# Kernel optimization log

Measured on AMD Instinct MI355X. Metric: run time of the kernel, lower is better.

Reference implementation:

```python
import jax, jax.numpy as jnp
import numpy as np

N, E = 50000, 800000
IN_C, HID_C, OUT_C, HEADS = 128, 32, 16, 4
NEG_SLOPE = 0.2


def gat_conv(x, src, dst, W, att_src, att_dst, bias, heads, out_ch, concat, n_nodes):
    # linear transform: [N, heads, out_ch]
    h = (x @ W).reshape(n_nodes, heads, out_ch)
    # per-node attention logits [N, heads]
    a_s = (h * att_src).sum(-1)
    a_d = (h * att_dst).sum(-1)
    # per-edge raw attention (edge j->i uses src logit of j, dst logit of i)
    alpha = jax.nn.leaky_relu(a_s[src] + a_d[dst], negative_slope=NEG_SLOPE)  # [E, heads]
    # segment softmax over destination neighborhoods
    amax = jax.ops.segment_max(alpha, dst, num_segments=n_nodes)
    ex = jnp.exp(alpha - amax[dst])
    den = jax.ops.segment_sum(ex, dst, num_segments=n_nodes)
    coef = ex / den[dst]  # [E, heads]
    # weighted scatter-add aggregation
    msg = h[src] * coef[:, :, None]  # [E, heads, out_ch]
    out = jax.ops.segment_sum(msg, dst, num_segments=n_nodes)  # [N, heads, out_ch]
    out = out.reshape(n_nodes, heads * out_ch) if concat else out.mean(axis=1)
    return out + bias


def setup_inputs() -> dict:
    key = jax.random.key(0)
    ks = jax.random.split(key, 10)
    x = jax.random.normal(ks[0], (N, IN_C), dtype=jnp.float32)
    edge_index = jax.random.randint(ks[1], (2, E), 0, N, dtype=jnp.int64)
    s1 = 1.0 / np.sqrt(IN_C)
    s2 = 1.0 / np.sqrt(HID_C * HEADS)
    W1 = jax.random.normal(ks[2], (IN_C, HEADS * HID_C), dtype=jnp.float32) * s1
    att_src1 = jax.random.normal(ks[3], (HEADS, HID_C), dtype=jnp.float32) * s1
    att_dst1 = jax.random.normal(ks[4], (HEADS, HID_C), dtype=jnp.float32) * s1
    b1 = jnp.zeros((HEADS * HID_C,), dtype=jnp.float32)
    W2 = jax.random.normal(ks[5], (HEADS * HID_C, OUT_C), dtype=jnp.float32) * s2
    att_src2 = jax.random.normal(ks[6], (1, OUT_C), dtype=jnp.float32) * s2
    att_dst2 = jax.random.normal(ks[7], (1, OUT_C), dtype=jnp.float32) * s2
    b2 = jnp.zeros((OUT_C,), dtype=jnp.float32)
    return {"x": x, "edge_index": edge_index, "W1": W1, "att_src1": att_src1,
            "att_dst1": att_dst1, "b1": b1, "W2": W2, "att_src2": att_src2,
            "att_dst2": att_dst2, "b2": b2}


def reference(x, edge_index, W1, att_src1, att_dst1, b1, W2, att_src2, att_dst2, b2):
    n = x.shape[0]
    # PyG GATConv default: add self loops
    ar = jnp.arange(n, dtype=edge_index.dtype)
    src = jnp.concatenate([edge_index[0], ar])
    dst = jnp.concatenate([edge_index[1], ar])
    h = gat_conv(x, src, dst, W1, att_src1, att_dst1, b1, HEADS, HID_C, True, n)
    h = jax.nn.elu(h)
    out = gat_conv(h, src, dst, W2, att_src2, att_dst2, b2, 1, OUT_C, False, n)
    return out
```

## Files before the change

### kernel.cpp

```cpp
#include <hip/hip_runtime.h>

typedef __attribute__((ext_vector_type(8))) short short8;
typedef __attribute__((ext_vector_type(4))) float f32x4;
typedef __attribute__((ext_vector_type(2))) float f32x2;

__device__ __forceinline__ float lrelu02(float a) { return a > 0.0f ? a : 0.2f * a; }

__device__ __forceinline__ unsigned bf16rne(float f) {
    unsigned u = __float_as_uint(f);
    return (u + 0x7fffu + ((u >> 16) & 1u)) >> 16;
}

__global__ __launch_bounds__(256) void k_rank(
    const int* __restrict__ ei, int* __restrict__ deg, int* __restrict__ rank, int E)
{
    int tid = blockIdx.x * blockDim.x + threadIdx.x;
    int nthr = gridDim.x * blockDim.x;
    int E4 = E & ~3;
    for (int b = tid * 4; b < E4; b += nthr * 4) {
        int4 d = *(const int4*)(ei + E + b);
        int4 r;
        r.x = atomicAdd(&deg[d.x], 1);
        r.y = atomicAdd(&deg[d.y], 1);
        r.z = atomicAdd(&deg[d.z], 1);
        r.w = atomicAdd(&deg[d.w], 1);
        *(int4*)(rank + b) = r;
    }
    for (int e = E4 + tid; e < E; e += nthr)
        rank[e] = atomicAdd(&deg[ei[E + e]], 1);
}

__global__ __launch_bounds__(256) void k_gemm1(
    const float* __restrict__ x, const float* __restrict__ W,
    const float* __restrict__ attS, const float* __restrict__ attD,
    unsigned short* __restrict__ h1, float* __restrict__ as1, float* __restrict__ ad1,
    int4* __restrict__ degz, int n4, int N)
{
    __shared__ unsigned short Wt[128 * 128];
    __shared__ unsigned short xs[64 * 128];

    const int t = threadIdx.x;
    const int lane = t & 63;
    const int wv = t >> 6;
    const int ln = lane & 15;
    const int lg = lane >> 4;
    const int r0 = blockIdx.x * 64;

    for (int i = blockIdx.x * 256 + t; i < n4; i += gridDim.x * 256)
        degz[i] = make_int4(0, 0, 0, 0);

    #pragma unroll
    for (int i = 0; i < 16; ++i) {
        int flat = i * 256 + t;
        int n = flat & 127;
        int k0 = (flat >> 7) * 4;
        float v0 = W[(size_t)(k0 + 0) * 128 + n];
        float v1 = W[(size_t)(k0 + 1) * 128 + n];
        float v2 = W[(size_t)(k0 + 2) * 128 + n];
        float v3 = W[(size_t)(k0 + 3) * 128 + n];
        uint2 pk;
        pk.x = bf16rne(v0) | (bf16rne(v1) << 16);
        pk.y = bf16rne(v2) | (bf16rne(v3) << 16);
        int byteo = n * 256 + ((k0 * 2) ^ ((n & 7) << 4));
        *(uint2*)((char*)Wt + byteo) = pk;
    }
    {
        int mbase = t >> 5, k0 = (t & 31) * 4;
        #pragma unroll
        for (int it = 0; it < 8; ++it) {
            int m = mbase + it * 8;
            int rr = r0 + m;
            float4 v = make_float4(0.f, 0.f, 0.f, 0.f);
            if (rr < N) v = *(const float4*)&x[(size_t)rr * 128 + k0];
            unsigned lo = bf16rne(v.x) | (bf16rne(v.y) << 16);
            unsigned hi = bf16rne(v.z) | (bf16rne(v.w) << 16);
            int byteo = m * 256 + ((k0 * 2) ^ ((m & 7) << 4));
            *(uint2*)((char*)xs + byteo) = make_uint2(lo, hi);
        }
    }
    __syncthreads();

    f32x4 acc[8];
    #pragma unroll
    for (int i = 0; i < 8; ++i) acc[i] = (f32x4)(0.f);

    #pragma unroll
    for (int kk = 0; kk < 4; ++kk) {
        int kb = (kk * 32 + lg * 8) * 2;
        int am = wv * 16 + ln;
        short8 a = *(const short8*)((char*)xs + am * 256 + (kb ^ ((am & 7) << 4)));
        #pragma unroll
        for (int tile = 0; tile < 8; ++tile) {
            int n = tile * 16 + ln;
            short8 b = *(const short8*)((char*)Wt + n * 256 + (kb ^ ((n & 7) << 4)));
            acc[tile] = __builtin_amdgcn_mfma_f32_16x16x32_bf16(a, b, acc[tile], 0, 0, 0);
        }
    }

    float aSt[8], aDt[8];
    #pragma unroll
    for (int tile = 0; tile < 8; ++tile) {
        aSt[tile] = attS[tile * 16 + ln];
        aDt[tile] = attD[tile * 16 + ln];
    }
    #pragma unroll
    for (int r = 0; r < 4; ++r) {
        int row = r0 + wv * 16 + lg * 4 + r;
        #pragma unroll
        for (int h = 0; h < 4; ++h) {
            float s = acc[2*h][r] * aSt[2*h] + acc[2*h+1][r] * aSt[2*h+1];
            float d = acc[2*h][r] * aDt[2*h] + acc[2*h+1][r] * aDt[2*h+1];
            s += __shfl_xor(s, 1); s += __shfl_xor(s, 2); s += __shfl_xor(s, 4); s += __shfl_xor(s, 8);
            d += __shfl_xor(d, 1); d += __shfl_xor(d, 2); d += __shfl_xor(d, 4); d += __shfl_xor(d, 8);
            if (ln == h * 4 + r && row < N) {
                as1[row * 4 + h] = s;
                ad1[row * 4 + h] = d;
            }
        }
    }

    __syncthreads();
    #pragma unroll
    for (int tile = 0; tile < 8; ++tile) {
        #pragma unroll
        for (int r = 0; r < 4; ++r) {
            int m = wv * 16 + lg * 4 + r;
            int byteo = m * 256 + (((tile * 16 + ln) * 2) ^ ((m & 7) << 4));
            *(unsigned short*)((char*)xs + byteo) = (unsigned short)bf16rne(acc[tile][r]);
        }
    }
    __syncthreads();
    #pragma unroll
    for (int it = 0; it < 4; ++it) {
        int idx = t + it * 256;
        int m = idx >> 4, o = idx & 15;
        int byteo = m * 256 + ((o * 16) ^ ((m & 7) << 4));
        if (r0 + m < N)
            *(uint4*)((char*)(h1 + (size_t)(r0 + m) * 128) + o * 16) =
                *(const uint4*)((const char*)xs + byteo);
    }
}

__global__ __launch_bounds__(256) void k_scan_local(
    const int* __restrict__ deg, int* __restrict__ rowptr, int* __restrict__ bsum, int N)
{
    const int t = threadIdx.x;
    const int base = blockIdx.x * 2048 + t * 8;
    int v[8];
    int s = 0;
    #pragma unroll
    for (int j = 0; j < 8; ++j) {
        int idx = base + j;
        v[j] = (idx < N) ? deg[idx] : 0;
        s += v[j];
    }
    __shared__ int ts[256];
    ts[t] = s;
    __syncthreads();
    #pragma unroll
    for (int off = 1; off < 256; off <<= 1) {
        int u = (t >= off) ? ts[t - off] : 0;
        __syncthreads();
        ts[t] += u;
        __syncthreads();
    }
    int ex = (t == 0) ? 0 : ts[t - 1];
    #pragma unroll
    for (int j = 0; j < 8; ++j) {
        int idx = base + j;
        if (idx < N) rowptr[idx] = ex;
        ex += v[j];
    }
    if (t == 255) bsum[blockIdx.x] = ts[255];
}

__global__ __launch_bounds__(256) void k_scan_add(
    int* __restrict__ rowptr, const int* __restrict__ bsum, int N, int E)
{
    const int t = threadIdx.x;
    __shared__ int soff;
    if (t < 64) {
        int v = (t < (int)blockIdx.x) ? bsum[t] : 0;
        #pragma unroll
        for (int m = 32; m >= 1; m >>= 1) v += __shfl_xor(v, m);
        if (t == 0) soff = v;
    }
    __syncthreads();
    int off = soff;
    const int base = blockIdx.x * 2048 + t * 8;
    #pragma unroll
    for (int j = 0; j < 8; ++j) {
        int idx = base + j;
        if (idx < N) rowptr[idx] += off;
    }
    if (blockIdx.x == 0 && t == 0) rowptr[N] = E;
}

__global__ __launch_bounds__(256) void k_fill2(const int* __restrict__ ei,
                                               const int* __restrict__ rank,
                                               const int* __restrict__ rowptr,
                                               int* __restrict__ col, int E) {
    int tid = blockIdx.x * blockDim.x + threadIdx.x;
    int nthr = gridDim.x * blockDim.x;
    int E4 = E & ~3;
    for (int b = tid * 4; b < E4; b += nthr * 4) {
        int4 d = *(const int4*)(ei + E + b);
        int4 s = *(const int4*)(ei + b);
        int4 r = *(const int4*)(rank + b);
        col[rowptr[d.x] + r.x] = s.x;
        col[rowptr[d.y] + r.y] = s.y;
        col[rowptr[d.z] + r.z] = s.z;
        col[rowptr[d.w] + r.w] = s.w;
    }
    for (int e = E4 + tid; e < E; e += nthr)
        col[rowptr[ei[E + e]] + rank[e]] = ei[e];
}

__global__ __launch_bounds__(256) void k_agg1(
    const unsigned short* __restrict__ h1, const float* __restrict__ as1,
    const float* __restrict__ ad1, const int* __restrict__ rowptr,
    const int* __restrict__ col, const float* __restrict__ b1,
    unsigned short* __restrict__ out1, int N)
{
    int wid = (int)(((unsigned)blockIdx.x * blockDim.x + threadIdx.x) >> 6);
    if (wid >= N) return;
    int lane = threadIdx.x & 63;
    int start = rowptr[wid], end = rowptr[wid + 1];
    int deg = end - start;
    const float4 ad = *(const float4*)(ad1 + (size_t)wid * 4);
    int head = lane >> 4;
    float adh = head == 0 ? ad.x : head == 1 ? ad.y : head == 2 ? ad.z : ad.w;

    float aself = as1[(size_t)wid * 4 + head];
    float vself = __expf(lrelu02(aself + adh));
    unsigned hvs = *(const unsigned*)(h1 + (size_t)wid * 128 + lane * 2);

    f32x2 acc2 = (f32x2)(0.f);

    if (deg <= 64) {
        int idx = lane & 15;
        float ex[4];
        int sv[4];
        float den = 0.f;
        #pragma unroll
        for (int b = 0; b < 4; ++b) {
            int j = b * 16 + idx;
            float v = 0.f;
            int sc = 0;
            if (j < deg) {
                sc = col[start + j];
                v = __expf(lrelu02(as1[(size_t)sc * 4 + head] + adh));
            }
            sv[b] = sc;
            ex[b] = v;
            den += v;
        }
        den += __shfl_xor(den, 1); den += __shfl_xor(den, 2);
        den += __shfl_xor(den, 4); den += __shfl_xor(den, 8);
        den += vself;
        float rden = 1.f / den;
        #pragma unroll
        for (int b = 0; b < 4; ++b) ex[b] *= rden;
        {
            float cs = vself * rden;
            f32x2 hs;
            hs.x = __uint_as_float(hvs << 16);
            hs.y = __uint_as_float(hvs & 0xffff0000u);
            acc2 += (f32x2)(cs) * hs;
        }
        int srcbase = lane & 48;

        #pragma unroll
        for (int b = 0; b < 4; ++b) {
            int rem = deg - b * 16;
            if (rem <= 0) break;
            if (rem >= 16) {
                int sq[16]; float cf[16]; unsigned hv[16];
                #pragma unroll
                for (int q = 0; q < 16; ++q) {
                    sq[q] = __builtin_amdgcn_readlane(sv[b], q);
                    cf[q] = __shfl(ex[b], srcbase | q);
                }
                #pragma unroll
                for (int q = 0; q < 16; ++q)
                    hv[q] = *(const unsigned*)(h1 + (size_t)sq[q] * 128 + lane * 2);
                #pragma unroll
                for (int q = 0; q < 16; ++q) {
                    f32x2 h2v;
                    h2v.x = __uint_as_float(hv[q] << 16);
                    h2v.y = __uint_as_float(hv[q] & 0xffff0000u);
                    acc2 += (f32x2)(cf[q]) * h2v;
                }
            } else {
                #pragma unroll
                for (int c4 = 0; c4 < 4; ++c4) {
                    if (c4 * 4 >= rem) break;
                    int sq[4]; float cf[4]; unsigned hv[4];
                    #pragma unroll
                    for (int jj = 0; jj < 4; ++jj) {
                        int q = c4 * 4 + jj;
                        sq[jj] = __builtin_amdgcn_readlane(sv[b], q);
                        cf[jj] = __shfl(ex[b], srcbase | q);
                    }
                    #pragma unroll
                    for (int jj = 0; jj < 4; ++jj)
                        hv[jj] = *(const unsigned*)(h1 + (size_t)sq[jj] * 128 + lane * 2);
                    #pragma unroll
                    for (int jj = 0; jj < 4; ++jj) {
                        f32x2 h2v;
                        h2v.x = __uint_as_float(hv[jj] << 16);
                        h2v.y = __uint_as_float(hv[jj] & 0xffff0000u);
                        acc2 += (f32x2)(cf[jj]) * h2v;
                    }
                }
            }
        }
    } else {
        float den0 = 0.f, den1 = 0.f, den2 = 0.f, den3 = 0.f;
        for (int e = start + lane; e < end; e += 64) {
            int src = col[e];
            const float4 a = *(const float4*)(as1 + (size_t)src * 4);
            den0 += __expf(lrelu02(a.x + ad.x));
            den1 += __expf(lrelu02(a.y + ad.y));
            den2 += __expf(lrelu02(a.z + ad.z));
            den3 += __expf(lrelu02(a.w + ad.w));
        }
        #pragma unroll
        for (int m = 32; m >= 1; m >>= 1) {
            den0 += __shfl_xor(den0, m); den1 += __shfl_xor(den1, m);
            den2 += __shfl_xor(den2, m); den3 += __shfl_xor(den3, m);
        }
        const float4 asf = *(const float4*)(as1 + (size_t)wid * 4);
        den0 += __expf(lrelu02(asf.x + ad.x));
        den1 += __expf(lrelu02(asf.y + ad.y));
        den2 += __expf(lrelu02(asf.z + ad.z));
        den3 += __expf(lrelu02(asf.w + ad.w));
        float rden = head == 0 ? 1.f/den0 : head == 1 ? 1.f/den1 : head == 2 ? 1.f/den2 : 1.f/den3;
        {
            float cs = vself * rden;
            f32x2 hs;
            hs.x = __uint_as_float(hvs << 16);
            hs.y = __uint_as_float(hvs & 0xffff0000u);
            acc2 += (f32x2)(cs) * hs;
        }
        for (int e = start; e < end; e += 8) {
            int sq[8]; float av[8], km[8]; unsigned hv[8];
            #pragma unroll
            for (int j = 0; j < 8; ++j) {
                int ee = e + j;
                bool ok = ee < end;
                int es = ok ? ee : e;
                sq[j] = __builtin_amdgcn_readfirstlane(col[es]);
                km[j] = ok ? 1.f : 0.f;
            }
            #pragma unroll
            for (int j = 0; j < 8; ++j)
                av[j] = as1[(size_t)sq[j] * 4 + head];
            #pragma unroll
            for (int j = 0; j < 8; ++j)
                hv[j] = *(const unsigned*)(h1 + (size_t)sq[j] * 128 + lane * 2);
            #pragma unroll
            for (int j = 0; j < 8; ++j) {
                float coef = km[j] * __expf(lrelu02(av[j] + adh)) * rden;
                f32x2 h2v;
                h2v.x = __uint_as_float(hv[j] << 16);
                h2v.y = __uint_as_float(hv[j] & 0xffff0000u);
                acc2 += (f32x2)(coef) * h2v;
            }
        }
    }

    int c0 = lane * 2;
    float o0 = acc2.x + b1[c0];
    float o1 = acc2.y + b1[c0 + 1];
    o0 = o0 > 0.f ? o0 : expm1f(o0);
    o1 = o1 > 0.f ? o1 : expm1f(o1);
    unsigned ov = bf16rne(o0) | (bf16rne(o1) << 16);
    *(unsigned*)((char*)out1 + (size_t)wid * 256 + lane * 4) = ov;
}

__global__ __launch_bounds__(256) void k_gemm2(
    const unsigned short* __restrict__ in, const float* __restrict__ W,
    const float* __restrict__ attS, const float* __restrict__ attD,
    float* __restrict__ h2, float* __restrict__ as2, float* __restrict__ ad2, int N)
{
    __shared__ unsigned short Wt[16 * 128];
    __shared__ unsigned short xs[64 * 128];
    const int t = threadIdx.x;
    const int lane = t & 63;
    const int wv = t >> 6;
    const int ln = lane & 15;
    const int lg = lane >> 4;
    const int r0 = blockIdx.x * 64;

    #pragma unroll
    for (int i = 0; i < 2; ++i) {
        int flat = i * 256 + t;
        int n = flat & 15;
        int k0 = (flat >> 4) * 4;
        float v0 = W[(size_t)(k0 + 0) * 16 + n];
        float v1 = W[(size_t)(k0 + 1) * 16 + n];
        float v2 = W[(size_t)(k0 + 2) * 16 + n];
        float v3 = W[(size_t)(k0 + 3) * 16 + n];
        uint2 pk;
        pk.x = bf16rne(v0) | (bf16rne(v1) << 16);
        pk.y = bf16rne(v2) | (bf16rne(v3) << 16);
        int byteo = n * 256 + ((k0 * 2) ^ ((n & 7) << 4));
        *(uint2*)((char*)Wt + byteo) = pk;
    }
    #pragma unroll
    for (int it = 0; it < 4; ++it) {
        int idx = t + it * 256;
        int m = idx >> 4, o = idx & 15;
        int rr = r0 + m;
        uint4 v = make_uint4(0, 0, 0, 0);
        if (rr < N) v = *(const uint4*)((const char*)(in + (size_t)rr * 128) + o * 16);
        int byteo = m * 256 + ((o * 16) ^ ((m & 7) << 4));
        *(uint4*)((char*)xs + byteo) = v;
    }
    __syncthreads();

    f32x4 acc = (f32x4)(0.f);
    #pragma unroll
    for (int kk = 0; kk < 4; ++kk) {
        int kb = (kk * 32 + lg * 8) * 2;
        int am = wv * 16 + ln;
        short8 a = *(const short8*)((char*)xs + am * 256 + (kb ^ ((am & 7) << 4)));
        short8 b = *(const short8*)((char*)Wt + ln * 256 + (kb ^ ((ln & 7) << 4)));
        acc = __builtin_amdgcn_mfma_f32_16x16x32_bf16(a, b, acc, 0, 0, 0);
    }

    float aSv = attS[ln], aDv = attD[ln];
    #pragma unroll
    for (int r = 0; r < 4; ++r) {
        int row = r0 + wv * 16 + lg * 4 + r;
        float s = acc[r] * aSv;
        float d = acc[r] * aDv;
        s += __shfl_xor(s, 1); s += __shfl_xor(s, 2); s += __shfl_xor(s, 4); s += __shfl_xor(s, 8);
        d += __shfl_xor(d, 1); d += __shfl_xor(d, 2); d += __shfl_xor(d, 4); d += __shfl_xor(d, 8);
        if (row < N) {
            h2[(size_t)row * 16 + ln] = acc[r];
            if (ln == 0) { as2[row] = s; ad2[row] = d; }
        }
    }
}

__global__ __launch_bounds__(256) void k_agg2(
    const float* __restrict__ h2, const float* __restrict__ as2,
    const float* __restrict__ ad2, const int* __restrict__ rowptr,
    const int* __restrict__ col, const float* __restrict__ b2,
    float* __restrict__ out, int N)
{
    int wid = (int)(((unsigned)blockIdx.x * blockDim.x + threadIdx.x) >> 6);
    if (wid >= N) return;
    int lane = threadIdx.x & 63;
    int start = rowptr[wid], end = rowptr[wid + 1];
    int deg = end - start;
    float adv = ad2[wid];
    int sub = lane >> 4, c = lane & 15;
    float vself = __expf(lrelu02(as2[wid] + adv));
    float acc = 0.f;

    if (deg <= 64) {
        float ex0 = 0.f;
        if (lane < deg) ex0 = __expf(lrelu02(as2[col[start + lane]] + adv));
        float den = ex0;
        #pragma unroll
        for (int m = 32; m >= 1; m >>= 1) den += __shfl_xor(den, m);
        den += vself;
        float rden = 1.f / den;
        ex0 *= rden;
        if (sub == 0) acc = fmaf(vself * rden, h2[(size_t)wid * 16 + c], acc);
        #pragma unroll
        for (int g = 0; g < 4; ++g) {
            if (g * 16 >= deg) break;
            int s[4]; float cf[4], hv[4];
            #pragma unroll
            for (int jj = 0; jj < 4; ++jj) {
                int j = g * 16 + jj * 4 + sub;
                s[jj]  = col[start + (j < deg ? j : 0)];
                cf[jj] = __shfl(ex0, j);
            }
            #pragma unroll
            for (int jj = 0; jj < 4; ++jj)
                hv[jj] = h2[(size_t)s[jj] * 16 + c];
            #pragma unroll
            for (int jj = 0; jj < 4; ++jj)
                acc = fmaf(cf[jj], hv[jj], acc);
        }
    } else {
        float den = 0.f;
        for (int e = start + lane; e < end; e += 64)
            den += __expf(lrelu02(as2[col[e]] + adv));
        #pragma unroll
        for (int m = 32; m >= 1; m >>= 1) den += __shfl_xor(den, m);
        den += vself;
        float rden = 1.f / den;
        if (sub == 0) acc = fmaf(vself * rden, h2[(size_t)wid * 16 + c], acc);
        for (int e0 = start + sub; e0 < end; e0 += 16) {
            int s[4]; float av[4], km[4], hv[4];
            #pragma unroll
            for (int jj = 0; jj < 4; ++jj) {
                int ee = e0 + jj * 4;
                bool ok = ee < end;
                int es = ok ? ee : e0;
                s[jj]  = col[es];
                km[jj] = ok ? 1.f : 0.f;
            }
            #pragma unroll
            for (int jj = 0; jj < 4; ++jj)
                av[jj] = as2[s[jj]];
            #pragma unroll
            for (int jj = 0; jj < 4; ++jj)
                hv[jj] = h2[(size_t)s[jj] * 16 + c];
            #pragma unroll
            for (int jj = 0; jj < 4; ++jj) {
                float coef = km[jj] * __expf(lrelu02(av[jj] + adv)) * rden;
                acc = fmaf(coef, hv[jj], acc);
            }
        }
    }

    acc += __shfl_xor(acc, 16);
    acc += __shfl_xor(acc, 32);
    if (lane < 16) out[(size_t)wid * 16 + lane] = acc + b2[lane];
}

extern "C" void kernel_launch(void* const* d_in, const int* in_sizes, int n_in,
                              void* d_out, int out_size, void* d_ws, size_t ws_size,
                              hipStream_t stream)
{
    const float* x   = (const float*)d_in[0];
    const int*   ei  = (const int*)d_in[1];
    const float* W1  = (const float*)d_in[2];
    const float* aS1 = (const float*)d_in[3];
    const float* aD1 = (const float*)d_in[4];
    const float* b1  = (const float*)d_in[5];
    const float* W2  = (const float*)d_in[6];
    const float* aS2 = (const float*)d_in[7];
    const float* aD2 = (const float*)d_in[8];
    const float* b2  = (const float*)d_in[9];
    float* out = (float*)d_out;

    int N = in_sizes[0] / 128;
    int E = in_sizes[1] / 2;
    int nblk = (N + 2047) / 2048;
    int G1 = (N + 63) / 64;

    char* w = (char*)d_ws;
    auto alloc = [&](size_t bytes) -> void* {
        void* p = (void*)w;
        w += (bytes + 255) & ~(size_t)255;
        return p;
    };
    unsigned short* h1   = (unsigned short*)alloc((size_t)N * 128 * 2);
    unsigned short* out1 = (unsigned short*)alloc((size_t)N * 128 * 2);
    float* as1   = (float*)alloc((size_t)N * 4 * 4);
    float* ad1   = (float*)alloc((size_t)N * 4 * 4);
    float* h2    = (float*)alloc((size_t)N * 16 * 4);
    float* as2v  = (float*)alloc((size_t)N * 4);
    float* ad2v  = (float*)alloc((size_t)N * 4);
    int* deg     = (int*)alloc((size_t)(N + 4) * 4);
    int* rowptr  = (int*)alloc((size_t)(N + 1) * 4);
    int* rank    = (int*)alloc((size_t)E * 4);
    int* col     = (int*)alloc((size_t)E * 4);
    int* bsum    = (int*)alloc(64 * 4);

    const int tb = 256;
    int n4 = (N + 3) / 4;

    k_gemm1<<<G1, tb, 0, stream>>>(x, W1, aS1, aD1, h1, as1, ad1,
                                   (int4*)deg, n4, N);
    k_rank <<<2048, tb, 0, stream>>>(ei, deg, rank, E);
    k_scan_local<<<nblk, tb, 0, stream>>>(deg, rowptr, bsum, N);
    k_scan_add  <<<nblk, tb, 0, stream>>>(rowptr, bsum, N, E);
    k_fill2<<<1024, tb, 0, stream>>>(ei, rank, rowptr, col, E);

    k_agg1 <<<(N + 3) / 4, tb, 0, stream>>>(h1, as1, ad1, rowptr, col, b1, out1, N);
    k_gemm2<<<G1, tb, 0, stream>>>(out1, W2, aS2, aD2, h2, as2v, ad2v, N);
    k_agg2 <<<(N + 3) / 4, tb, 0, stream>>>(h2, as2v, ad2v, rowptr, col, b2, out, N);
}
```

Baseline: 150.1 us.

## Fuse CSR build stages into one kernel with inter-block flag synchronization

```diff
diff --git a/kernel.cpp b/kernel.cpp
--- a/kernel.cpp
+++ b/kernel.cpp
@@ -11,30 +11,127 @@
     return (u + 0x7fffu + ((u >> 16) & 1u)) >> 16;
 }
 
-__global__ __launch_bounds__(256) void k_rank(
-    const int* __restrict__ ei, int* __restrict__ deg, int* __restrict__ rank, int E)
+__device__ __forceinline__ void waitflag(int* f, int target) {
+    while (__hip_atomic_load(f, __ATOMIC_ACQUIRE, __HIP_MEMORY_SCOPE_AGENT) < target)
+        __builtin_amdgcn_s_sleep(8);
+}
+
+__global__ __launch_bounds__(256, 8) void k_csr(
+    const int* __restrict__ ei, int* __restrict__ deg, int* __restrict__ rank,
+    int* __restrict__ rowptr, int* __restrict__ bsum, int* __restrict__ col,
+    int* __restrict__ flags, int E, int N, int RB, int SB)
 {
-    int tid = blockIdx.x * blockDim.x + threadIdx.x;
-    int nthr = gridDim.x * blockDim.x;
-    int E4 = E & ~3;
-    for (int b = tid * 4; b < E4; b += nthr * 4) {
-        int4 d = *(const int4*)(ei + E + b);
-        int4 r;
-        r.x = atomicAdd(&deg[d.x], 1);
-        r.y = atomicAdd(&deg[d.y], 1);
-        r.z = atomicAdd(&deg[d.z], 1);
-        r.w = atomicAdd(&deg[d.w], 1);
-        *(int4*)(rank + b) = r;
-    }
-    for (int e = E4 + tid; e < E; e += nthr)
-        rank[e] = atomicAdd(&deg[ei[E + e]], 1);
+    const int t = threadIdx.x;
+    const int b = blockIdx.x;
+
+    if (b < RB) {
+        int tid = b * 256 + t;
+        int nthr = RB * 256;
+        int E4 = E & ~3;
+        for (int e = tid * 4; e < E4; e += nthr * 4) {
+            int4 d = *(const int4*)(ei + E + e);
+            int4 r;
+            r.x = atomicAdd(&deg[d.x], 1);
+            r.y = atomicAdd(&deg[d.y], 1);
+            r.z = atomicAdd(&deg[d.z], 1);
+            r.w = atomicAdd(&deg[d.w], 1);
+            *(int4*)(rank + e) = r;
+        }
+        for (int e = E4 + tid; e < E; e += nthr)
+            rank[e] = atomicAdd(&deg[ei[E + e]], 1);
+        __syncthreads();
+        if (t == 0) {
+            __threadfence();
+            __hip_atomic_fetch_add(&flags[0], 1, __ATOMIC_RELEASE, __HIP_MEMORY_SCOPE_AGENT);
+        }
+        return;
+    }
+
+    if (b < RB + SB) {
+        const int sb = b - RB;
+        if (t == 0) waitflag(&flags[0], RB);
+        __syncthreads();
+
+        const int base = sb * 2048 + t * 8;
+        int v[8];
+        int s = 0;
+        #pragma unroll
+        for (int j = 0; j < 8; ++j) {
+            int idx = base + j;
+            v[j] = (idx < N) ? deg[idx] : 0;
+            s += v[j];
+        }
+        __shared__ int ts[256];
+        ts[t] = s;
+        __syncthreads();
+        #pragma unroll
+        for (int off = 1; off < 256; off <<= 1) {
+            int u = (t >= off) ? ts[t - off] : 0;
+            __syncthreads();
+            ts[t] += u;
+            __syncthreads();
+        }
+        int myex = (t == 0) ? 0 : ts[t - 1];
+        if (t == 255) bsum[sb] = ts[255];
+        __syncthreads();
+        if (t == 0) {
+            __threadfence();
+            __hip_atomic_fetch_add(&flags[1], 1, __ATOMIC_RELEASE, __HIP_MEMORY_SCOPE_AGENT);
+            waitflag(&flags[1], SB);
+        }
+        __syncthreads();
+
+        __shared__ int soff;
+        if (t < 64) {
+            int u = (t < sb) ? bsum[t] : 0;
+            #pragma unroll
+            for (int m = 32; m >= 1; m >>= 1) u += __shfl_xor(u, m);
+            if (t == 0) soff = u;
+        }
+        __syncthreads();
+        int run = soff + myex;
+        #pragma unroll
+        for (int j = 0; j < 8; ++j) {
+            int idx = base + j;
+            if (idx < N) rowptr[idx] = run;
+            run += v[j];
+        }
+        if (sb == 0 && t == 0) rowptr[N] = E;
+        __syncthreads();
+        if (t == 0) {
+            __threadfence();
+            __hip_atomic_fetch_add(&flags[2], 1, __ATOMIC_RELEASE, __HIP_MEMORY_SCOPE_AGENT);
+        }
+        return;
+    }
+
+    if (t == 0) waitflag(&flags[2], SB);
+    __syncthreads();
+    {
+        int fb = b - RB - SB;
+        int FB = gridDim.x - RB - SB;
+        int tid = fb * 256 + t;
+        int nthr = FB * 256;
+        int E4 = E & ~3;
+        for (int e = tid * 4; e < E4; e += nthr * 4) {
+            int4 d = *(const int4*)(ei + E + e);
+            int4 sv = *(const int4*)(ei + e);
+            int4 r = *(const int4*)(rank + e);
+            col[rowptr[d.x] + r.x] = sv.x;
+            col[rowptr[d.y] + r.y] = sv.y;
+            col[rowptr[d.z] + r.z] = sv.z;
+            col[rowptr[d.w] + r.w] = sv.w;
+        }
+        for (int e = E4 + tid; e < E; e += nthr)
+            col[rowptr[ei[E + e]] + rank[e]] = ei[e];
+    }
 }
 
 __global__ __launch_bounds__(256) void k_gemm1(
     const float* __restrict__ x, const float* __restrict__ W,
     const float* __restrict__ attS, const float* __restrict__ attD,
     unsigned short* __restrict__ h1, float* __restrict__ as1, float* __restrict__ ad1,
-    int4* __restrict__ degz, int n4, int N)
+    int4* __restrict__ degz, int* __restrict__ flags, int n4, int N)
 {
     __shared__ unsigned short Wt[128 * 128];
     __shared__ unsigned short xs[64 * 128];
@@ -48,6 +145,7 @@
 
     for (int i = blockIdx.x * 256 + t; i < n4; i += gridDim.x * 256)
         degz[i] = make_int4(0, 0, 0, 0);
+    if (blockIdx.x == 0 && t < 8) flags[t] = 0;
 
     #pragma unroll
     for (int i = 0; i < 16; ++i) {
@@ -139,81 +237,6 @@
             *(uint4*)((char*)(h1 + (size_t)(r0 + m) * 128) + o * 16) =
                 *(const uint4*)((const char*)xs + byteo);
     }
-}
-
-__global__ __launch_bounds__(256) void k_scan_local(
-    const int* __restrict__ deg, int* __restrict__ rowptr, int* __restrict__ bsum, int N)
-{
-    const int t = threadIdx.x;
-    const int base = blockIdx.x * 2048 + t * 8;
-    int v[8];
-    int s = 0;
-    #pragma unroll
-    for (int j = 0; j < 8; ++j) {
-        int idx = base + j;
-        v[j] = (idx < N) ? deg[idx] : 0;
-        s += v[j];
-    }
-    __shared__ int ts[256];
-    ts[t] = s;
-    __syncthreads();
-    #pragma unroll
-    for (int off = 1; off < 256; off <<= 1) {
-        int u = (t >= off) ? ts[t - off] : 0;
-        __syncthreads();
-        ts[t] += u;
-        __syncthreads();
-    }
-    int ex = (t == 0) ? 0 : ts[t - 1];
-    #pragma unroll
-    for (int j = 0; j < 8; ++j) {
-        int idx = base + j;
-        if (idx < N) rowptr[idx] = ex;
-        ex += v[j];
-    }
-    if (t == 255) bsum[blockIdx.x] = ts[255];
-}
-
-__global__ __launch_bounds__(256) void k_scan_add(
-    int* __restrict__ rowptr, const int* __restrict__ bsum, int N, int E)
-{
-    const int t = threadIdx.x;
-    __shared__ int soff;
-    if (t < 64) {
-        int v = (t < (int)blockIdx.x) ? bsum[t] : 0;
-        #pragma unroll
-        for (int m = 32; m >= 1; m >>= 1) v += __shfl_xor(v, m);
-        if (t == 0) soff = v;
-    }
-    __syncthreads();
-    int off = soff;
-    const int base = blockIdx.x * 2048 + t * 8;
-    #pragma unroll
-    for (int j = 0; j < 8; ++j) {
-        int idx = base + j;
-        if (idx < N) rowptr[idx] += off;
-    }
-    if (blockIdx.x == 0 && t == 0) rowptr[N] = E;
-}
-
-__global__ __launch_bounds__(256) void k_fill2(const int* __restrict__ ei,
-                                               const int* __restrict__ rank,
-                                               const int* __restrict__ rowptr,
-                                               int* __restrict__ col, int E) {
-    int tid = blockIdx.x * blockDim.x + threadIdx.x;
-    int nthr = gridDim.x * blockDim.x;
-    int E4 = E & ~3;
-    for (int b = tid * 4; b < E4; b += nthr * 4) {
-        int4 d = *(const int4*)(ei + E + b);
-        int4 s = *(const int4*)(ei + b);
-        int4 r = *(const int4*)(rank + b);
-        col[rowptr[d.x] + r.x] = s.x;
-        col[rowptr[d.y] + r.y] = s.y;
-        col[rowptr[d.z] + r.z] = s.z;
-        col[rowptr[d.w] + r.w] = s.w;
-    }
-    for (int e = E4 + tid; e < E; e += nthr)
-        col[rowptr[ei[E + e]] + rank[e]] = ei[e];
 }
 
 __global__ __launch_bounds__(256) void k_agg1(
@@ -565,17 +588,18 @@
     int* rank    = (int*)alloc((size_t)E * 4);
     int* col     = (int*)alloc((size_t)E * 4);
     int* bsum    = (int*)alloc(64 * 4);
+    int* flags   = (int*)alloc(8 * 4);
 
     const int tb = 256;
     int n4 = (N + 3) / 4;
+    const int RB = 800;
+    const int SB = nblk;
+    const int FB = 455;
 
     k_gemm1<<<G1, tb, 0, stream>>>(x, W1, aS1, aD1, h1, as1, ad1,
-                                   (int4*)deg, n4, N);
-    k_rank <<<2048, tb, 0, stream>>>(ei, deg, rank, E);
-    k_scan_local<<<nblk, tb, 0, stream>>>(deg, rowptr, bsum, N);
-    k_scan_add  <<<nblk, tb, 0, stream>>>(rowptr, bsum, N, E);
-    k_fill2<<<1024, tb, 0, stream>>>(ei, rank, rowptr, col, E);
-
+                                   (int4*)deg, flags, n4, N);
+    k_csr  <<<RB + SB + FB, tb, 0, stream>>>(ei, deg, rank, rowptr, bsum, col,
+                                             flags, E, N, RB, SB);
     k_agg1 <<<(N + 3) / 4, tb, 0, stream>>>(h1, as1, ad1, rowptr, col, b1, out1, N);
     k_gemm2<<<G1, tb, 0, stream>>>(out1, W2, aS2, aD2, h2, as2v, ad2v, N);
     k_agg2 <<<(N + 3) / 4, tb, 0, stream>>>(h2, as2v, ad2v, rowptr, col, b2, out, N);
```

Result: slower. 276.5 us (+84.2%).
